# Kernel tuning notes

Hardware: AMD Instinct MI355X
Metric: run time of the kernel (lower is better)

Reference implementation:

```python
import jax, jax.numpy as jnp
import numpy as np

B, T, P, NI = 16, 365, 10, 8      # batch, timesteps, producers, injectors
EP, EI = 90, 80                   # p2p and i2p edge counts
PD, ID, ED = 10, 8, 10            # feature dims
H, L = 128, 3                     # gnn hidden, gnn layers
LH, DH = 256, 64                  # lstm hidden, decoder hidden


def setup_inputs() -> dict:
    key = jax.random.key(0)
    ks = jax.random.split(key, 24)
    def rn(i, sh, s=1.0):
        return jax.random.normal(ks[i], sh, dtype=jnp.float32) * s
    s = 0.05
    inp = {
        'producer_features': rn(0, (B, T, P, PD)),
        'injector_features': rn(1, (B, T, NI, ID)),
        'edge_features_p2p': rn(2, (B, T, EP, ED)),
        'edge_features_i2p': rn(3, (B, T, EI, ED)),
        'edge_index_p2p': jax.random.randint(ks[4], (2, EP), 0, P),
        'edge_index_i2p': jax.random.randint(ks[5], (2, EI), 0, NI),
        # GNN encoders
        'Wpe': rn(6, (PD, H), s), 'bpe': jnp.zeros((H,), jnp.float32),
        'Wie': rn(7, (ID, H), s), 'bie': jnp.zeros((H,), jnp.float32),
        'Wep': rn(8, (ED, H), s), 'bep': jnp.zeros((H,), jnp.float32),
        'Wei': rn(9, (ED, H), s), 'bei': jnp.zeros((H,), jnp.float32),
        # GNN message/update weights, stacked over L layers
        'Wmp': rn(10, (L, 2 * H, H), s), 'bmp': jnp.zeros((L, H), jnp.float32),
        'Wmi': rn(11, (L, 2 * H, H), s), 'bmi': jnp.zeros((L, H), jnp.float32),
        'Wu': rn(12, (L, 3 * H, H), s), 'bu': jnp.zeros((L, H), jnp.float32),
        # 2-layer LSTM (gate order i,f,g,o)
        'Wx0': rn(13, (P * H, 4 * LH), s), 'Wh0': rn(14, (LH, 4 * LH), s), 'lb0': jnp.zeros((4 * LH,), jnp.float32),
        'Wx1': rn(15, (LH, 4 * LH), s), 'Wh1': rn(16, (LH, 4 * LH), s), 'lb1': jnp.zeros((4 * LH,), jnp.float32),
        # decoder MLP with PReLU
        'Wd1': rn(17, (LH, DH), s), 'bd1': jnp.zeros((DH,), jnp.float32), 'a1': jnp.float32(0.25),
        'Wd2': rn(18, (DH, DH), s), 'bd2': jnp.zeros((DH,), jnp.float32), 'a2': jnp.float32(0.25),
        'Wd3': rn(19, (DH, 2 * P), s), 'bd3': jnp.zeros((2 * P,), jnp.float32),
    }
    return inp


def _lstm_layer(x, Wx, Wh, b):
    # x: (B, T, D) -> (B, T, H_lstm)
    Bn = x.shape[0]
    Hn = Wh.shape[0]
    xs = jnp.swapaxes(x @ Wx + b, 0, 1)  # (T, B, 4H) input projections precomputed
    def step(carry, xt):
        h, c = carry
        z = xt + h @ Wh
        i, f, g, o = jnp.split(z, 4, axis=-1)
        c = jax.nn.sigmoid(f) * c + jax.nn.sigmoid(i) * jnp.tanh(g)
        h = jax.nn.sigmoid(o) * jnp.tanh(c)
        return (h, c), h
    init = (jnp.zeros((Bn, Hn), x.dtype), jnp.zeros((Bn, Hn), x.dtype))
    _, hs = jax.lax.scan(step, init, xs)
    return jnp.swapaxes(hs, 0, 1)


def _forward(pf, jf, ep, ei, ip2p, ii2p,
             Wpe, bpe, Wie, bie, Wep, bep, Wei, bei,
             Wmp, bmp, Wmi, bmi, Wu, bu,
             Wx0, Wh0, lb0, Wx1, Wh1, lb1,
             Wd1, bd1, a1, Wd2, bd2, a2, Wd3, bd3):
    relu = jax.nn.relu
    # node / edge encoders (all timesteps batched; identical math to per-t loop)
    h_p = relu(pf @ Wpe + bpe)   # (B,T,P,H)
    h_i = relu(jf @ Wie + bie)   # (B,T,NI,H)
    e_p = relu(ep @ Wep + bep)   # (B,T,EP,H)
    e_i = relu(ei @ Wei + bei)   # (B,T,EI,H)
    sp, dp = ip2p[0], ip2p[1]
    si, di = ii2p[0], ii2p[1]
    for l in range(Wmp.shape[0]):
        m_p = relu(jnp.concatenate([h_p[:, :, sp, :], e_p], -1) @ Wmp[l] + bmp[l])  # (B,T,EP,H)
        agg_p = jnp.zeros_like(h_p).at[:, :, dp, :].add(m_p)
        m_i = relu(jnp.concatenate([h_i[:, :, si, :], e_i], -1) @ Wmi[l] + bmi[l])  # (B,T,EI,H)
        agg_i = jnp.zeros_like(h_p).at[:, :, di, :].add(m_i)
        h_p = relu(jnp.concatenate([h_p, agg_p, agg_i], -1) @ Wu[l] + bu[l])
    emb = h_p                                        # (B,T,P,H) producer embeddings
    x = emb.reshape(emb.shape[0], emb.shape[1], -1)  # (B,T,P*H)
    h1 = _lstm_layer(x, Wx0, Wh0, lb0)
    h2 = _lstm_layer(h1, Wx1, Wh1, lb1)              # (B,T,LH)
    prelu = lambda v, a: jnp.where(v >= 0, v, a * v)
    d = prelu(h2 @ Wd1 + bd1, a1)
    d = prelu(d @ Wd2 + bd2, a2)
    rates = (d @ Wd3 + bd3).reshape(h2.shape[0], h2.shape[1], -1, 2)
    oil = jax.nn.softplus(rates[..., 0])
    water = jax.nn.softplus(rates[..., 1])
    return oil, water, emb


def reference(producer_features, injector_features, edge_features_p2p, edge_features_i2p,
              edge_index_p2p, edge_index_i2p,
              Wpe, bpe, Wie, bie, Wep, bep, Wei, bei,
              Wmp, bmp, Wmi, bmi, Wu, bu,
              Wx0, Wh0, lb0, Wx1, Wh1, lb1,
              Wd1, bd1, a1, Wd2, bd2, a2, Wd3, bd3):
    return _forward(producer_features, injector_features, edge_features_p2p, edge_features_i2p,
                    edge_index_p2p, edge_index_i2p,
                    Wpe, bpe, Wie, bie, Wep, bep, Wei, bei,
                    Wmp, bmp, Wmi, bmi, Wu, bu,
                    Wx0, Wh0, lb0, Wx1, Wh1, lb1,
                    Wd1, bd1, a1, Wd2, bd2, a2, Wd3, bd3)
```

## Files before the change

kernel.cpp:

```cpp
#include <hip/hip_runtime.h>

#define B_   16
#define T_   365
#define P_   10
#define NI_  8
#define EP_  90
#define EI_  80
#define PD_  10
#define ID_  8
#define ED_  10
#define H_   128
#define LH_  256
#define DH_  64
#define BT_  (B_*T_)
#define NPROW_ (BT_*P_)
#define NIROW_ (BT_*NI_)

typedef unsigned long long u64;
typedef __attribute__((ext_vector_type(8))) short short8b;
typedef __attribute__((ext_vector_type(4))) float f32x4;

#define MFMA_BF16(a,b,c) __builtin_amdgcn_mfma_f32_16x16x32_bf16(a,b,c,0,0,0)

__device__ __forceinline__ short f2bf(float f){
    union { float f; unsigned u; } a; a.f = f;
    unsigned r = a.u + 0x7fffu + ((a.u >> 16) & 1u);
    return (short)(r >> 16);
}

__device__ __forceinline__ short* lds_a(short* base, int row, int kbyte, int rowstrideB){
    return (short*)((char*)base + row*rowstrideB + (kbyte ^ ((row & 7) << 4)));
}
__device__ __forceinline__ void st_bf(short* base, int row, int col, int rowstrideB, short v){
    *(short*)((char*)base + row*rowstrideB + ((2*col) ^ ((row & 7) << 4))) = v;
}

#define WBF_TOTAL 352256
__global__ __launch_bounds__(512) void k_prep(
    const float* __restrict__ Wep, const float* __restrict__ Wei,
    const float* __restrict__ Wmp, const float* __restrict__ Wmi,
    const float* __restrict__ Wu,  short* __restrict__ wbf)
{
    int i = blockIdx.x*512 + threadIdx.x;
    if (i >= WBF_TOTAL) return;
    short v;
    if (i < 8192) {
        const float* W = (i < 4096) ? Wep : Wei;
        int j = i & 4095, c = j >> 5, k = j & 31;
        v = (k < PD_) ? f2bf(W[k*H_ + c]) : (short)0;
    } else if (i < 106496) {
        int j = i - 8192;
        const float* W = (j < 49152) ? Wmp : Wmi;
        j %= 49152;
        int l = j >> 14, r = j & 16383, c = r >> 7, k = r & 127;
        v = f2bf(W[l*2*H_*H_ + k*H_ + c]);
    } else if (i < 204800) {
        int j = i - 106496;
        const float* W = (j < 49152) ? Wmp : Wmi;
        j %= 49152;
        int l = j >> 14, r = j & 16383, c = r >> 7, k = r & 127;
        v = f2bf(W[l*2*H_*H_ + (H_ + k)*H_ + c]);
    } else {
        int j = i - 204800;
        int l = j / 49152, r = j % 49152, c = r / 384, k = r % 384;
        v = f2bf(Wu[l*3*H_*H_ + k*H_ + c]);
    }
    wbf[i] = v;
}

__global__ __launch_bounds__(512) void k_enc(
    const float* __restrict__ pf, const float* __restrict__ jf,
    const float* __restrict__ Wpe, const float* __restrict__ bpe,
    const float* __restrict__ Wie, const float* __restrict__ bie,
    float* __restrict__ hp, float* __restrict__ hi)
{
    const int sub = threadIdx.x >> 7;
    const int j   = threadIdx.x & 127;
    const int r   = blockIdx.x*4 + sub;
    __shared__ float xs[4][16];
    if (r < NPROW_) {
        if (j < PD_) xs[sub][j] = pf[(size_t)r*PD_ + j];
    } else {
        if (j < ID_) xs[sub][j] = jf[(size_t)(r - NPROW_)*ID_ + j];
    }
    __syncthreads();
    if (r < NPROW_) {
        float acc = bpe[j];
        #pragma unroll
        for (int k = 0; k < PD_; k++) acc += xs[sub][k]*Wpe[k*H_ + j];
        hp[(size_t)r*H_ + j] = fmaxf(acc, 0.f);
    } else {
        float acc = bie[j];
        #pragma unroll
        for (int k = 0; k < ID_; k++) acc += xs[sub][k]*Wie[k*H_ + j];
        hi[(size_t)(r - NPROW_)*H_ + j] = fmaxf(acc, 0.f);
    }
}

__device__ __forceinline__ void edge_phase(
    int bt, int tid, int wv, int ln15, int lg, int NE,
    const float* __restrict__ ef, const int* __restrict__ eidx,
    const short* __restrict__ WencT, const float* __restrict__ benc,
    const short* __restrict__ WbotT,
    const float* __restrict__ hproj_s, float* __restrict__ agg_s,
    short* __restrict__ eenc_A, short* __restrict__ raw_A,
    int* __restrict__ src_s, int* __restrict__ dst_s)
{
    for (int e = tid; e < NE; e += 512) { src_s[e] = eidx[e]; dst_s[e] = eidx[NE + e]; }

    const int c = 16*wv + ln15;
    const float bv = benc[c];

    for (int tb = 0; tb < NE; tb += 32) {
        const int RT = (NE - tb < 32) ? (NE - tb) : 32;
        __syncthreads();
        ((unsigned*)raw_A)[tid] = 0u;
        ((unsigned*)raw_A)[tid + 512] = 0u;
        __syncthreads();
        for (int i = tid; i < RT*ED_; i += 512) {
            const int e = i/ED_, k = i - e*ED_;
            st_bf(raw_A, e, k, 128, f2bf(ef[(size_t)bt*NE*ED_ + (tb + e)*ED_ + k]));
        }
        __syncthreads();
        #pragma unroll
        for (int rtl = 0; rtl < 2; rtl++) {
            short8b a = *(short8b*)lds_a(raw_A, 16*rtl + ln15, lg*16, 128);
            short8b b = *(const short8b*)&WencT[(size_t)c*32 + lg*8];
            f32x4 acc = {0.f,0.f,0.f,0.f};
            acc = MFMA_BF16(a, b, acc);
            #pragma unroll
            for (int j = 0; j < 4; j++) {
                const int row = 16*rtl + lg*4 + j;
                st_bf(eenc_A, row, c, 256, f2bf(fmaxf(acc[j] + bv, 0.f)));
            }
        }
        __syncthreads();
        f32x4 acc0 = {0.f,0.f,0.f,0.f}, acc1 = {0.f,0.f,0.f,0.f};
        #pragma unroll
        for (int kc = 0; kc < 4; kc++) {
            short8b b  = *(const short8b*)&WbotT[(size_t)c*128 + kc*32 + lg*8];
            short8b a0 = *(short8b*)lds_a(eenc_A, ln15,      kc*64 + lg*16, 256);
            short8b a1 = *(short8b*)lds_a(eenc_A, 16 + ln15, kc*64 + lg*16, 256);
            acc0 = MFMA_BF16(a0, b, acc0);
            acc1 = MFMA_BF16(a1, b, acc1);
        }
        #pragma unroll
        for (int j = 0; j < 4; j++) {
            const int el0 = lg*4 + j;
            if (el0 < RT) {
                const int e = tb + el0;
                const float m = fmaxf(acc0[j] + hproj_s[src_s[e]*H_ + c], 0.f);
                atomicAdd(&agg_s[dst_s[e]*H_ + c], m);
            }
            const int el1 = 16 + lg*4 + j;
            if (el1 < RT) {
                const int e = tb + el1;
                const float m = fmaxf(acc1[j] + hproj_s[src_s[e]*H_ + c], 0.f);
                atomicAdd(&agg_s[dst_s[e]*H_ + c], m);
            }
        }
    }
}

__global__ __launch_bounds__(512) void k_layer(
    int l,
    const float* __restrict__ hp_in, const float* __restrict__ hi_g,
    const int* __restrict__ ip2p, const int* __restrict__ ii2p,
    const float* __restrict__ epf, const float* __restrict__ eif,
    const short* __restrict__ wbf,
    const float* __restrict__ bep, const float* __restrict__ bei,
    const float* __restrict__ bmp, const float* __restrict__ bmi,
    const float* __restrict__ bu,
    float* __restrict__ hp_out)
{
    const int bt   = blockIdx.x;
    const int tid  = threadIdx.x;
    const int wv   = tid >> 6;
    const int lane = tid & 63;
    const int ln15 = lane & 15;
    const int lg   = lane >> 4;

    __shared__ short h_s[32*128];
    __shared__ float hpp_s[P_*H_];
    __shared__ float hip_s[NI_*H_];
    __shared__ float aggp_s[P_*H_];
    __shared__ float aggi_s[P_*H_];
    __shared__ short eenc_A[32*128];
    __shared__ short updA[16*384];
    __shared__ int   src_s[EP_], dst_s[EP_];
    short* raw_A = updA;

    const short* WencPT = wbf;
    const short* WencIT = wbf + 4096;
    const short* WtopPT = wbf + 8192   + l*16384;
    const short* WtopIT = wbf + 57344  + l*16384;
    const short* WbotPT = wbf + 106496 + l*16384;
    const short* WbotIT = wbf + 155648 + l*16384;
    const short* WuT    = wbf + 204800 + l*49152;
    const float* bmp_g = bmp + l*H_;
    const float* bmi_g = bmi + l*H_;
    const float* bu_g  = bu  + l*H_;

    for (int i = tid; i < P_*H_; i += 512) {
        const int r = i >> 7, c = i & 127;
        st_bf(h_s, r, c, 256, f2bf(hp_in[(size_t)bt*(P_*H_) + i]));
        aggp_s[i] = 0.f; aggi_s[i] = 0.f;
    }
    for (int i = tid; i < NI_*H_; i += 512) {
        const int r = i >> 7, c = i & 127;
        st_bf(h_s, 16 + r, c, 256, f2bf(hi_g[(size_t)bt*(NI_*H_) + i]));
    }
    __syncthreads();

    {
        f32x4 accp = {0.f,0.f,0.f,0.f}, acci = {0.f,0.f,0.f,0.f};
        const int c = 16*wv + ln15;
        #pragma unroll
        for (int kc = 0; kc < 4; kc++) {
            short8b ap = *(short8b*)lds_a(h_s, ln15,      kc*64 + lg*16, 256);
            short8b bp = *(const short8b*)&WtopPT[(size_t)c*128 + kc*32 + lg*8];
            accp = MFMA_BF16(ap, bp, accp);
            short8b ai = *(short8b*)lds_a(h_s, 16 + ln15, kc*64 + lg*16, 256);
            short8b bi = *(const short8b*)&WtopIT[(size_t)c*128 + kc*32 + lg*8];
            acci = MFMA_BF16(ai, bi, acci);
        }
        const float bpv = bmp_g[c], biv = bmi_g[c];
        #pragma unroll
        for (int j = 0; j < 4; j++) {
            const int r = lg*4 + j;
            if (r < P_)  hpp_s[r*H_ + c] = accp[j] + bpv;
            if (r < NI_) hip_s[r*H_ + c] = acci[j] + biv;
        }
    }
    __syncthreads();

    edge_phase(bt, tid, wv, ln15, lg, EP_, epf, ip2p, WencPT, bep, WbotPT,
               hpp_s, aggp_s, eenc_A, raw_A, src_s, dst_s);
    __syncthreads();
    edge_phase(bt, tid, wv, ln15, lg, EI_, eif, ii2p, WencIT, bei, WbotIT,
               hip_s, aggi_s, eenc_A, raw_A, src_s, dst_s);
    __syncthreads();

    for (int i = tid; i < P_*H_; i += 512) {
        const int r = i >> 7, c = i & 127;
        const short hv = *(short*)((char*)h_s + r*256 + ((2*c) ^ ((r & 7) << 4)));
        st_bf(updA, r, c,        768, hv);
        st_bf(updA, r, 128 + c,  768, f2bf(aggp_s[i]));
        st_bf(updA, r, 256 + c,  768, f2bf(aggi_s[i]));
    }
    __syncthreads();

    {
        f32x4 acc = {0.f,0.f,0.f,0.f};
        const int c = 16*wv + ln15;
        #pragma unroll
        for (int kc = 0; kc < 12; kc++) {
            short8b a = *(short8b*)lds_a(updA, ln15, kc*64 + lg*16, 768);
            short8b b = *(const short8b*)&WuT[(size_t)c*384 + kc*32 + lg*8];
            acc = MFMA_BF16(a, b, acc);
        }
        const float bv = bu_g[c];
        #pragma unroll
        for (int j = 0; j < 4; j++) {
            const int r = lg*4 + j;
            if (r < P_)
                hp_out[(size_t)bt*(P_*H_) + r*H_ + c] = fmaxf(acc[j] + bv, 0.f);
        }
    }
}

__global__ __launch_bounds__(256) void k_gemm_xp(
    const float* __restrict__ A, const float* __restrict__ W,
    const float* __restrict__ bias, float* __restrict__ C)
{
    const int m0 = blockIdx.x*32;
    const int n0 = blockIdx.y*128;
    const int tid = threadIdx.x;
    __shared__ float As[32*32];
    __shared__ float Ws[32*128];
    const int c0 = (tid & 31)*4;
    const int r0 = (tid >> 5)*4;
    float acc[4][4] = {};
    for (int kc = 0; kc < 1280; kc += 32) {
        for (int i = tid; i < 1024; i += 256) {
            const int r = i >> 5, k = i & 31, row = m0 + r;
            As[i] = (row < BT_) ? A[(size_t)row*1280 + kc + k] : 0.f;
        }
        for (int i = tid; i < 4096; i += 256) {
            const int kk = i >> 7, cc = i & 127;
            Ws[i] = W[(size_t)(kc + kk)*1024 + n0 + cc];
        }
        __syncthreads();
        #pragma unroll 8
        for (int j = 0; j < 32; j++) {
            const float4 wv = *(const float4*)&Ws[j*128 + c0];
            const float a0 = As[(r0    )*32 + j];
            const float a1 = As[(r0 + 1)*32 + j];
            const float a2 = As[(r0 + 2)*32 + j];
            const float a3 = As[(r0 + 3)*32 + j];
            acc[0][0]+=a0*wv.x; acc[0][1]+=a0*wv.y; acc[0][2]+=a0*wv.z; acc[0][3]+=a0*wv.w;
            acc[1][0]+=a1*wv.x; acc[1][1]+=a1*wv.y; acc[1][2]+=a1*wv.z; acc[1][3]+=a1*wv.w;
            acc[2][0]+=a2*wv.x; acc[2][1]+=a2*wv.y; acc[2][2]+=a2*wv.z; acc[2][3]+=a2*wv.w;
            acc[3][0]+=a3*wv.x; acc[3][1]+=a3*wv.y; acc[3][2]+=a3*wv.z; acc[3][3]+=a3*wv.w;
        }
        __syncthreads();
    }
    #pragma unroll
    for (int i = 0; i < 4; i++) {
        const int row = m0 + r0 + i;
        if (row < BT_) {
            float4 o;
            o.x = acc[i][0] + bias[n0 + c0 + 0];
            o.y = acc[i][1] + bias[n0 + c0 + 1];
            o.z = acc[i][2] + bias[n0 + c0 + 2];
            o.w = acc[i][3] + bias[n0 + c0 + 3];
            *(float4*)&C[(size_t)row*1024 + n0 + c0] = o;
        }
    }
}

__device__ __forceinline__ float sigm(float x) { return 1.f/(1.f + expf(-x)); }

__global__ __launch_bounds__(512) void k_lstm_scan(
    const float* __restrict__ xproj0,
    const float* __restrict__ Wh0,
    const float* __restrict__ Wx1, const float* __restrict__ Wh1,
    const float* __restrict__ lb1,
    float* __restrict__ h1_ex, float* __restrict__ h2_ex,
    float* __restrict__ h2_out,
    int* __restrict__ flag0, int* __restrict__ flag1)
{
    const int tid   = threadIdx.x;
    const int layer = blockIdx.x >> 5;
    const int s     = blockIdx.x & 31;
    const int cc    = tid & 31;
    const int g     = tid >> 5;
    const int gcol  = (cc >> 3)*256 + s*8 + (cc & 7);

    __shared__ float h_s[8192];
    __shared__ float red[16*544];
    __shared__ float z_s[16*33];

    float w[32];
    if (layer == 0) {
        #pragma unroll
        for (int j = 0; j < 16; j++) w[j] = Wh0[(size_t)(g*16 + j)*1024 + gcol];
    } else {
        #pragma unroll
        for (int j = 0; j < 32; j++) {
            const int k = g*32 + j;
            w[j] = (k < 256) ? Wx1[(size_t)k*1024 + gcol]
                             : Wh1[(size_t)(k - 256)*1024 + gcol];
        }
    }

    const int wj = tid >> 3, wb = (tid & 7)*2;
    float cst0 = 0.f, cst1 = 0.f;
    const float xv_l1 = lb1[gcol];

    const u64* ex1 = (const u64*)h1_ex;
    const u64* ex2 = (const u64*)h2_ex;

    for (int t = 0; t < T_; t++) {
        float xv;
        if (layer == 0) xv = xproj0[((size_t)g*T_ + t)*1024 + gcol];
        else            xv = xv_l1;

        if (layer == 0) {
            if (tid < 32 && tid != s)
                while (__hip_atomic_load(&flag0[tid], __ATOMIC_RELAXED, __HIP_MEMORY_SCOPE_AGENT) < t) {}
        } else {
            if (tid < 32) {
                while (__hip_atomic_load(&flag0[tid], __ATOMIC_RELAXED, __HIP_MEMORY_SCOPE_AGENT) < t + 1) {}
            } else if (tid < 64 && (tid - 32) != s) {
                while (__hip_atomic_load(&flag1[tid - 32], __ATOMIC_RELAXED, __HIP_MEMORY_SCOPE_AGENT) < t) {}
            }
        }
        __syncthreads();

        if (layer == 0) {
            #pragma unroll
            for (int i = 0; i < 4; i++) {
                const int idx = tid + i*512;
                u64 v = __hip_atomic_load(&ex1[(size_t)t*2048 + idx], __ATOMIC_RELAXED, __HIP_MEMORY_SCOPE_AGENT);
                *(u64*)&h_s[2*idx] = v;
            }
        } else {
            #pragma unroll
            for (int i = 0; i < 4; i++) {
                const int idx = tid + i*512;
                u64 v1 = __hip_atomic_load(&ex1[(size_t)(t + 1)*2048 + idx], __ATOMIC_RELAXED, __HIP_MEMORY_SCOPE_AGENT);
                u64 v2 = __hip_atomic_load(&ex2[(size_t)t*2048 + idx],       __ATOMIC_RELAXED, __HIP_MEMORY_SCOPE_AGENT);
                *(u64*)&h_s[2*idx]        = v1;
                *(u64*)&h_s[4096 + 2*idx] = v2;
            }
        }
        __syncthreads();

        float acc[16];
        #pragma unroll
        for (int i = 0; i < 16; i++) acc[i] = 0.f;
        if (layer == 0) {
            #pragma unroll
            for (int j = 0; j < 16; j++) {
                const float wv = w[j];
                const float4* hp4 = (const float4*)&h_s[(g*16 + j)*16];
                const float4 h0 = hp4[0], h1v = hp4[1], h2v = hp4[2], h3v = hp4[3];
                acc[0]+=h0.x*wv;  acc[1]+=h0.y*wv;  acc[2]+=h0.z*wv;  acc[3]+=h0.w*wv;
                acc[4]+=h1v.x*wv; acc[5]+=h1v.y*wv; acc[6]+=h1v.z*wv; acc[7]+=h1v.w*wv;
                acc[8]+=h2v.x*wv; acc[9]+=h2v.y*wv; acc[10]+=h2v.z*wv;acc[11]+=h2v.w*wv;
                acc[12]+=h3v.x*wv;acc[13]+=h3v.y*wv;acc[14]+=h3v.w*wv;acc[15]+=h3v.w*wv;
            }
        } else {
            #pragma unroll
            for (int j = 0; j < 32; j++) {
                const float wv = w[j];
                const float4* hp4 = (const float4*)&h_s[(g*32 + j)*16];
                const float4 h0 = hp4[0], h1v = hp4[1], h2v = hp4[2], h3v = hp4[3];
                acc[0]+=h0.x*wv;  acc[1]+=h0.y*wv;  acc[2]+=h0.z*wv;  acc[3]+=h0.w*wv;
                acc[4]+=h1v.x*wv; acc[5]+=h1v.y*wv; acc[6]+=h1v.z*wv; acc[7]+=h1v.w*wv;
                acc[8]+=h2v.x*wv; acc[9]+=h2v.y*wv; acc[10]+=h2v.z*wv;acc[11]+=h2v.w*wv;
                acc[12]+=h3v.x*wv;acc[13]+=h3v.y*wv;acc[14]+=h3v.z*wv;acc[15]+=h3v.w*wv;
            }
        }
        __syncthreads();
        {
            float* rp = &red[g*544 + cc*17];
            #pragma unroll
            for (int b = 0; b < 16; b++) rp[b] = acc[b];
        }
        __syncthreads();
        {
            float zsum = xv;
            #pragma unroll
            for (int g2 = 0; g2 < 16; g2++) zsum += red[g2*544 + cc*17 + g];
            z_s[g*33 + cc] = zsum;
        }
        __syncthreads();
        if (tid < 64) {
            const float zi0 = z_s[wb*33      + wj      ];
            const float zf0 = z_s[wb*33      + 8  + wj ];
            const float zg0 = z_s[wb*33      + 16 + wj ];
            const float zo0 = z_s[wb*33      + 24 + wj ];
            const float zi1 = z_s[(wb+1)*33  + wj      ];
            const float zf1 = z_s[(wb+1)*33  + 8  + wj ];
            const float zg1 = z_s[(wb+1)*33  + 16 + wj ];
            const float zo1 = z_s[(wb+1)*33  + 24 + wj ];
            cst0 = sigm(zf0)*cst0 + sigm(zi0)*tanhf(zg0);
            const float h0 = sigm(zo0)*tanhf(cst0);
            cst1 = sigm(zf1)*cst1 + sigm(zi1)*tanhf(zg1);
            const float h1o = sigm(zo1)*tanhf(cst1);
            union { float f[2]; u64 u; } pk;
            pk.f[0] = h0; pk.f[1] = h1o;
            u64* dst = (u64*)((layer == 0 ? h1_ex : h2_ex)
                              + (size_t)(t + 1)*4096 + (s*8 + wj)*16 + wb);
            __hip_atomic_store(dst, pk.u, __ATOMIC_RELAXED, __HIP_MEMORY_SCOPE_AGENT);
            if (layer == 1) {
                h2_out[((size_t)wb*T_     + t)*LH_ + s*8 + wj] = h0;
                h2_out[((size_t)(wb+1)*T_ + t)*LH_ + s*8 + wj] = h1o;
            }
        }
        asm volatile("s_waitcnt vmcnt(0)" ::: "memory");
        if (tid == 0) {
            int* f = (layer == 0) ? &flag0[s] : &flag1[s];
            __hip_atomic_store(f, t + 1, __ATOMIC_RELAXED, __HIP_MEMORY_SCOPE_AGENT);
        }
    }
}

__global__ __launch_bounds__(256) void k_dec(
    const float* __restrict__ h2,
    const float* __restrict__ Wd1, const float* __restrict__ bd1, const float* __restrict__ a1p,
    const float* __restrict__ Wd2, const float* __restrict__ bd2, const float* __restrict__ a2p,
    const float* __restrict__ Wd3, const float* __restrict__ bd3,
    float* __restrict__ oil, float* __restrict__ water)
{
    const int sub = threadIdx.x >> 6;
    const int tid = threadIdx.x & 63;
    const int r   = blockIdx.x*4 + sub;
    __shared__ float hrow[4][256], d1s[4][64], d2s[4][64];
    for (int i = tid; i < 256; i += 64) hrow[sub][i] = h2[(size_t)r*256 + i];
    __syncthreads();
    const float a1 = a1p[0], a2 = a2p[0];
    float acc = bd1[tid];
    for (int k = 0; k < 256; k++) acc += hrow[sub][k]*Wd1[k*64 + tid];
    d1s[sub][tid] = (acc >= 0.f) ? acc : a1*acc;
    __syncthreads();
    acc = bd2[tid];
    for (int k = 0; k < 64; k++) acc += d1s[sub][k]*Wd2[k*64 + tid];
    d2s[sub][tid] = (acc >= 0.f) ? acc : a2*acc;
    __syncthreads();
    if (tid < 20) {
        acc = bd3[tid];
        for (int k = 0; k < 64; k++) acc += d2s[sub][k]*Wd3[k*20 + tid];
        const float spv = (acc > 20.f) ? acc : log1pf(expf(acc));
        const int p = tid >> 1;
        if (tid & 1) water[(size_t)r*10 + p] = spv;
        else         oil  [(size_t)r*10 + p] = spv;
    }
}

extern "C" void kernel_launch(void* const* d_in, const int* in_sizes, int n_in,
                              void* d_out, int out_size, void* d_ws, size_t ws_size,
                              hipStream_t stream)
{
    const float* pf  = (const float*)d_in[0];
    const float* jf  = (const float*)d_in[1];
    const float* epf = (const float*)d_in[2];
    const float* eif = (const float*)d_in[3];
    const int*   ip2p= (const int*)d_in[4];
    const int*   ii2p= (const int*)d_in[5];
    const float* Wpe = (const float*)d_in[6];  const float* bpe = (const float*)d_in[7];
    const float* Wie = (const float*)d_in[8];  const float* bie = (const float*)d_in[9];
    const float* Wep = (const float*)d_in[10]; const float* bep = (const float*)d_in[11];
    const float* Wei = (const float*)d_in[12]; const float* bei = (const float*)d_in[13];
    const float* Wmp = (const float*)d_in[14]; const float* bmp = (const float*)d_in[15];
    const float* Wmi = (const float*)d_in[16]; const float* bmi = (const float*)d_in[17];
    const float* Wu  = (const float*)d_in[18]; const float* bu  = (const float*)d_in[19];
    const float* Wx0 = (const float*)d_in[20]; const float* Wh0 = (const float*)d_in[21];
    const float* lb0 = (const float*)d_in[22];
    const float* Wx1 = (const float*)d_in[23]; const float* Wh1 = (const float*)d_in[24];
    const float* lb1 = (const float*)d_in[25];
    const float* Wd1 = (const float*)d_in[26]; const float* bd1 = (const float*)d_in[27];
    const float* a1  = (const float*)d_in[28];
    const float* Wd2 = (const float*)d_in[29]; const float* bd2 = (const float*)d_in[30];
    const float* a2  = (const float*)d_in[31];
    const float* Wd3 = (const float*)d_in[32]; const float* bd3 = (const float*)d_in[33];

    float* oil   = (float*)d_out;
    float* water = oil + NPROW_;
    float* emb   = water + NPROW_;

    float* ws    = (float*)d_ws;
    float* X0    = ws;
    float* X1    = X0 + 7475200;
    float* hibuf = X1 + 7475200;
    float* xp0   = hibuf + 5980160;
    float* h1ex  = xp0 + 5980160;
    float* h2ex  = h1ex + 1499136;
    float* h2o   = h2ex + 1499136;
    int*   flag0 = (int*)(h2o + 1495040);
    int*   flag1 = flag0 + 32;
    short* wbf   = (short*)(flag0 + 64);

    hipMemsetAsync(flag0, 0, 64*sizeof(int), stream);
    hipMemsetAsync(h1ex, 0, 4096*sizeof(float), stream);
    hipMemsetAsync(h2ex, 0, 4096*sizeof(float), stream);

    k_prep<<<(WBF_TOTAL + 511)/512, 512, 0, stream>>>(Wep, Wei, Wmp, Wmi, Wu, wbf);

    k_enc<<<(NPROW_ + NIROW_)/4, 512, 0, stream>>>(pf, jf, Wpe, bpe, Wie, bie, X0, hibuf);

    k_layer<<<BT_, 512, 0, stream>>>(0, X0, hibuf, ip2p, ii2p, epf, eif,
        wbf, bep, bei, bmp, bmi, bu, X1);
    k_layer<<<BT_, 512, 0, stream>>>(1, X1, hibuf, ip2p, ii2p, epf, eif,
        wbf, bep, bei, bmp, bmi, bu, X0);
    k_layer<<<BT_, 512, 0, stream>>>(2, X0, hibuf, ip2p, ii2p, epf, eif,
        wbf, bep, bei, bmp, bmi, bu, emb);

    dim3 gx((BT_ + 31)/32, 8);
    k_gemm_xp<<<gx, 256, 0, stream>>>(emb, Wx0, lb0, xp0);

    k_lstm_scan<<<64, 512, 0, stream>>>(xp0, Wh0, Wx1, Wh1, lb1,
                                        h1ex, h2ex, h2o, flag0, flag1);

    k_dec<<<BT_/4, 256, 0, stream>>>(h2o, Wd1, bd1, a1, Wd2, bd2, a2, Wd3, bd3, oil, water);
}
```

Measured before the change: 5.068 ms.

## Use poison-value polling in LSTM scan and bf16 MFMA for input projection

The LSTM scan no longer uses per-block flag counters. Each consumer now spins directly on the exchanged hidden-state words, which are pre-filled with a poison pattern, so one barrier and the vmcnt wait plus flag store are removed from every timestep. The input-projection GEMM is rewritten to use bf16 MFMA with a pre-transposed bf16 copy of Wx0 made in the prep kernel, replacing the fp32 FMA tiling. A wrong accumulator index (h3v.w used where h3v.z belonged) is also fixed. The costs are extra memset traffic over both exchange buffers, bf16 rounding in the projection, and the assumption that real hidden values never equal the poison pattern.

```diff
diff --git a/kernel.cpp b/kernel.cpp
--- a/kernel.cpp
+++ b/kernel.cpp
@@ -21,6 +21,7 @@
 typedef __attribute__((ext_vector_type(4))) float f32x4;
 
 #define MFMA_BF16(a,b,c) __builtin_amdgcn_mfma_f32_16x16x32_bf16(a,b,c,0,0,0)
+#define POIS64 0x7F7F7F7F7F7F7F7FULL
 
 __device__ __forceinline__ short f2bf(float f){
     union { float f; unsigned u; } a; a.f = f;
@@ -35,11 +36,13 @@
     *(short*)((char*)base + row*rowstrideB + ((2*col) ^ ((row & 7) << 4))) = v;
 }
 
-#define WBF_TOTAL 352256
+#define WXT_OFF  352256
+#define WBF_TOTAL (352256 + 1310720)
 __global__ __launch_bounds__(512) void k_prep(
     const float* __restrict__ Wep, const float* __restrict__ Wei,
     const float* __restrict__ Wmp, const float* __restrict__ Wmi,
-    const float* __restrict__ Wu,  short* __restrict__ wbf)
+    const float* __restrict__ Wu,  const float* __restrict__ Wx0,
+    short* __restrict__ wbf)
 {
     int i = blockIdx.x*512 + threadIdx.x;
     if (i >= WBF_TOTAL) return;
@@ -60,10 +63,14 @@
         j %= 49152;
         int l = j >> 14, r = j & 16383, c = r >> 7, k = r & 127;
         v = f2bf(W[l*2*H_*H_ + (H_ + k)*H_ + c]);
-    } else {
+    } else if (i < WXT_OFF) {
         int j = i - 204800;
         int l = j / 49152, r = j % 49152, c = r / 384, k = r % 384;
         v = f2bf(Wu[l*3*H_*H_ + k*H_ + c]);
+    } else {
+        int j = i - WXT_OFF;
+        int c = j / 1280, k = j % 1280;
+        v = f2bf(Wx0[(size_t)k*1024 + c]);
     }
     wbf[i] = v;
 }
@@ -269,57 +276,51 @@
     }
 }
 
-__global__ __launch_bounds__(256) void k_gemm_xp(
-    const float* __restrict__ A, const float* __restrict__ W,
+__global__ __launch_bounds__(512) void k_gemm_xp(
+    const float* __restrict__ A, const short* __restrict__ WxT,
     const float* __restrict__ bias, float* __restrict__ C)
 {
     const int m0 = blockIdx.x*32;
-    const int n0 = blockIdx.y*128;
+    const int n0 = blockIdx.y*64;
     const int tid = threadIdx.x;
-    __shared__ float As[32*32];
-    __shared__ float Ws[32*128];
-    const int c0 = (tid & 31)*4;
-    const int r0 = (tid >> 5)*4;
-    float acc[4][4] = {};
-    for (int kc = 0; kc < 1280; kc += 32) {
-        for (int i = tid; i < 1024; i += 256) {
-            const int r = i >> 5, k = i & 31, row = m0 + r;
-            As[i] = (row < BT_) ? A[(size_t)row*1280 + kc + k] : 0.f;
-        }
-        for (int i = tid; i < 4096; i += 256) {
-            const int kk = i >> 7, cc = i & 127;
-            Ws[i] = W[(size_t)(kc + kk)*1024 + n0 + cc];
-        }
-        __syncthreads();
-        #pragma unroll 8
-        for (int j = 0; j < 32; j++) {
-            const float4 wv = *(const float4*)&Ws[j*128 + c0];
-            const float a0 = As[(r0    )*32 + j];
-            const float a1 = As[(r0 + 1)*32 + j];
-            const float a2 = As[(r0 + 2)*32 + j];
-            const float a3 = As[(r0 + 3)*32 + j];
-            acc[0][0]+=a0*wv.x; acc[0][1]+=a0*wv.y; acc[0][2]+=a0*wv.z; acc[0][3]+=a0*wv.w;
-            acc[1][0]+=a1*wv.x; acc[1][1]+=a1*wv.y; acc[1][2]+=a1*wv.z; acc[1][3]+=a1*wv.w;
-            acc[2][0]+=a2*wv.x; acc[2][1]+=a2*wv.y; acc[2][2]+=a2*wv.z; acc[2][3]+=a2*wv.w;
-            acc[3][0]+=a3*wv.x; acc[3][1]+=a3*wv.y; acc[3][2]+=a3*wv.z; acc[3][3]+=a3*wv.w;
-        }
-        __syncthreads();
-    }
+    const int wv = tid >> 6, lane = tid & 63;
+    const int ln15 = lane & 15, lg = lane >> 4;
+    const int wr = wv >> 2, wc = wv & 3;
+    const int c = n0 + wc*16 + ln15;
+
+    __shared__ short As[32*64];
+
+    f32x4 acc = {0.f,0.f,0.f,0.f};
+    for (int kc0 = 0; kc0 < 1280; kc0 += 64) {
+        #pragma unroll
+        for (int i = 0; i < 4; i++) {
+            const int o = tid + i*512;
+            const int row = o >> 6, k = o & 63;
+            const int grow = m0 + row;
+            const float av = (grow < BT_) ? A[(size_t)grow*1280 + kc0 + k] : 0.f;
+            st_bf(As, row, k, 128, f2bf(av));
+        }
+        __syncthreads();
+        #pragma unroll
+        for (int h = 0; h < 2; h++) {
+            short8b a = *(short8b*)lds_a(As, wr*16 + ln15, h*64 + lg*16, 128);
+            short8b b = *(const short8b*)&WxT[(size_t)c*1280 + kc0 + h*32 + lg*8];
+            acc = MFMA_BF16(a, b, acc);
+        }
+        __syncthreads();
+    }
+    const float bv = bias[c];
     #pragma unroll
-    for (int i = 0; i < 4; i++) {
-        const int row = m0 + r0 + i;
-        if (row < BT_) {
-            float4 o;
-            o.x = acc[i][0] + bias[n0 + c0 + 0];
-            o.y = acc[i][1] + bias[n0 + c0 + 1];
-            o.z = acc[i][2] + bias[n0 + c0 + 2];
-            o.w = acc[i][3] + bias[n0 + c0 + 3];
-            *(float4*)&C[(size_t)row*1024 + n0 + c0] = o;
-        }
+    for (int j = 0; j < 4; j++) {
+        const int grow = m0 + wr*16 + lg*4 + j;
+        if (grow < BT_) C[(size_t)grow*1024 + c] = acc[j] + bv;
     }
 }
 
 __device__ __forceinline__ float sigm(float x) { return 1.f/(1.f + expf(-x)); }
+__device__ __forceinline__ u64 ald(const u64* p){
+    return __hip_atomic_load(p, __ATOMIC_RELAXED, __HIP_MEMORY_SCOPE_AGENT);
+}
 
 __global__ __launch_bounds__(512) void k_lstm_scan(
     const float* __restrict__ xproj0,
@@ -327,8 +328,7 @@
     const float* __restrict__ Wx1, const float* __restrict__ Wh1,
     const float* __restrict__ lb1,
     float* __restrict__ h1_ex, float* __restrict__ h2_ex,
-    float* __restrict__ h2_out,
-    int* __restrict__ flag0, int* __restrict__ flag1)
+    float* __restrict__ h2_out)
 {
     const int tid   = threadIdx.x;
     const int layer = blockIdx.x >> 5;
@@ -367,32 +367,38 @@
         else            xv = xv_l1;
 
         if (layer == 0) {
-            if (tid < 32 && tid != s)
-                while (__hip_atomic_load(&flag0[tid], __ATOMIC_RELAXED, __HIP_MEMORY_SCOPE_AGENT) < t) {}
+            const u64* base = ex1 + (size_t)t*2048;
+            u64 v[4];
+            #pragma unroll
+            for (int i = 0; i < 4; i++) v[i] = ald(base + tid + i*512);
+            for (;;) {
+                bool ok = true;
+                #pragma unroll
+                for (int i = 0; i < 4; i++)
+                    if (v[i] == POIS64) { v[i] = ald(base + tid + i*512); ok = false; }
+                if (ok) break;
+            }
+            #pragma unroll
+            for (int i = 0; i < 4; i++) *(u64*)&h_s[2*(tid + i*512)] = v[i];
         } else {
-            if (tid < 32) {
-                while (__hip_atomic_load(&flag0[tid], __ATOMIC_RELAXED, __HIP_MEMORY_SCOPE_AGENT) < t + 1) {}
-            } else if (tid < 64 && (tid - 32) != s) {
-                while (__hip_atomic_load(&flag1[tid - 32], __ATOMIC_RELAXED, __HIP_MEMORY_SCOPE_AGENT) < t) {}
-            }
-        }
-        __syncthreads();
-
-        if (layer == 0) {
+            const u64* b1 = ex1 + (size_t)(t + 1)*2048;
+            const u64* b2 = ex2 + (size_t)t*2048;
+            u64 v1[4], v2[4];
+            #pragma unroll
+            for (int i = 0; i < 4; i++) { v1[i] = ald(b1 + tid + i*512); v2[i] = ald(b2 + tid + i*512); }
+            for (;;) {
+                bool ok = true;
+                #pragma unroll
+                for (int i = 0; i < 4; i++) {
+                    if (v1[i] == POIS64) { v1[i] = ald(b1 + tid + i*512); ok = false; }
+                    if (v2[i] == POIS64) { v2[i] = ald(b2 + tid + i*512); ok = false; }
+                }
+                if (ok) break;
+            }
             #pragma unroll
             for (int i = 0; i < 4; i++) {
-                const int idx = tid + i*512;
-                u64 v = __hip_atomic_load(&ex1[(size_t)t*2048 + idx], __ATOMIC_RELAXED, __HIP_MEMORY_SCOPE_AGENT);
-                *(u64*)&h_s[2*idx] = v;
-            }
-        } else {
-            #pragma unroll
-            for (int i = 0; i < 4; i++) {
-                const int idx = tid + i*512;
-                u64 v1 = __hip_atomic_load(&ex1[(size_t)(t + 1)*2048 + idx], __ATOMIC_RELAXED, __HIP_MEMORY_SCOPE_AGENT);
-                u64 v2 = __hip_atomic_load(&ex2[(size_t)t*2048 + idx],       __ATOMIC_RELAXED, __HIP_MEMORY_SCOPE_AGENT);
-                *(u64*)&h_s[2*idx]        = v1;
-                *(u64*)&h_s[4096 + 2*idx] = v2;
+                *(u64*)&h_s[2*(tid + i*512)]        = v1[i];
+                *(u64*)&h_s[4096 + 2*(tid + i*512)] = v2[i];
             }
         }
         __syncthreads();
@@ -409,7 +415,7 @@
                 acc[0]+=h0.x*wv;  acc[1]+=h0.y*wv;  acc[2]+=h0.z*wv;  acc[3]+=h0.w*wv;
                 acc[4]+=h1v.x*wv; acc[5]+=h1v.y*wv; acc[6]+=h1v.z*wv; acc[7]+=h1v.w*wv;
                 acc[8]+=h2v.x*wv; acc[9]+=h2v.y*wv; acc[10]+=h2v.z*wv;acc[11]+=h2v.w*wv;
-                acc[12]+=h3v.x*wv;acc[13]+=h3v.y*wv;acc[14]+=h3v.w*wv;acc[15]+=h3v.w*wv;
+                acc[12]+=h3v.x*wv;acc[13]+=h3v.y*wv;acc[14]+=h3v.z*wv;acc[15]+=h3v.w*wv;
             }
         } else {
             #pragma unroll
@@ -423,13 +429,13 @@
                 acc[12]+=h3v.x*wv;acc[13]+=h3v.y*wv;acc[14]+=h3v.z*wv;acc[15]+=h3v.w*wv;
             }
         }
-        __syncthreads();
         {
             float* rp = &red[g*544 + cc*17];
             #pragma unroll
             for (int b = 0; b < 16; b++) rp[b] = acc[b];
         }
         __syncthreads();
+
         {
             float zsum = xv;
             #pragma unroll
@@ -437,6 +443,7 @@
             z_s[g*33 + cc] = zsum;
         }
         __syncthreads();
+
         if (tid < 64) {
             const float zi0 = z_s[wb*33      + wj      ];
             const float zf0 = z_s[wb*33      + 8  + wj ];
@@ -459,11 +466,6 @@
                 h2_out[((size_t)wb*T_     + t)*LH_ + s*8 + wj] = h0;
                 h2_out[((size_t)(wb+1)*T_ + t)*LH_ + s*8 + wj] = h1o;
             }
-        }
-        asm volatile("s_waitcnt vmcnt(0)" ::: "memory");
-        if (tid == 0) {
-            int* f = (layer == 0) ? &flag0[s] : &flag1[s];
-            __hip_atomic_store(f, t + 1, __ATOMIC_RELAXED, __HIP_MEMORY_SCOPE_AGENT);
         }
     }
 }
@@ -539,15 +541,14 @@
     float* h1ex  = xp0 + 5980160;
     float* h2ex  = h1ex + 1499136;
     float* h2o   = h2ex + 1499136;
-    int*   flag0 = (int*)(h2o + 1495040);
-    int*   flag1 = flag0 + 32;
-    short* wbf   = (short*)(flag0 + 64);
-
-    hipMemsetAsync(flag0, 0, 64*sizeof(int), stream);
+    short* wbf   = (short*)(h2o + 1495040);
+
+    hipMemsetAsync(h1ex, 0x7F, 1499136*sizeof(float), stream);
+    hipMemsetAsync(h2ex, 0x7F, 1499136*sizeof(float), stream);
     hipMemsetAsync(h1ex, 0, 4096*sizeof(float), stream);
     hipMemsetAsync(h2ex, 0, 4096*sizeof(float), stream);
 
-    k_prep<<<(WBF_TOTAL + 511)/512, 512, 0, stream>>>(Wep, Wei, Wmp, Wmi, Wu, wbf);
+    k_prep<<<(WBF_TOTAL + 511)/512, 512, 0, stream>>>(Wep, Wei, Wmp, Wmi, Wu, Wx0, wbf);
 
     k_enc<<<(NPROW_ + NIROW_)/4, 512, 0, stream>>>(pf, jf, Wpe, bpe, Wie, bie, X0, hibuf);
 
@@ -558,11 +559,10 @@
     k_layer<<<BT_, 512, 0, stream>>>(2, X0, hibuf, ip2p, ii2p, epf, eif,
         wbf, bep, bei, bmp, bmi, bu, emb);
 
-    dim3 gx((BT_ + 31)/32, 8);
-    k_gemm_xp<<<gx, 256, 0, stream>>>(emb, Wx0, lb0, xp0);
-
-    k_lstm_scan<<<64, 512, 0, stream>>>(xp0, Wh0, Wx1, Wh1, lb1,
-                                        h1ex, h2ex, h2o, flag0, flag1);
+    dim3 gx((BT_ + 31)/32, 1024/64);
+    k_gemm_xp<<<gx, 512, 0, stream>>>(emb, wbf + WXT_OFF, lb0, xp0);
+
+    k_lstm_scan<<<64, 512, 0, stream>>>(xp0, Wh0, Wx1, Wh1, lb1, h1ex, h2ex, h2o);
 
     k_dec<<<BT_/4, 256, 0, stream>>>(h2o, Wd1, bd1, a1, Wd2, bd2, a2, Wd3, bd3, oil, water);
 }
```

Result: faster. 4.427 ms (-12.6%).
